# Kernel tuning notes

Measured on AMD Instinct MI355X. Metric: run time of the kernel, lower is better.

## Reference

```python
import jax, jax.numpy as jnp
import numpy as np

EMB = 1024
HEADS = 16
HEAD_DIM = EMB // HEADS
FF = 4 * EMB
EPS = 1e-5


def gelu_tanh(x):
    c = jnp.sqrt(jnp.asarray(2.0 / jnp.pi, dtype=x.dtype))
    return 0.5 * x * (1.0 + jnp.tanh(c * (x + 0.044715 * x ** 3)))


def layernorm(x, scale, bias):
    mean = jnp.mean(x, axis=-1, keepdims=True)
    # torch x.var() default is unbiased (ddof=1)
    var = jnp.var(x, axis=-1, keepdims=True, ddof=1)
    return (x - mean) / jnp.sqrt(var + EPS) * scale + bias


def setup_inputs() -> dict:
    key = jax.random.key(0)
    ks = jax.random.split(key, 12)
    s = lambda k, shape, sc=0.02: (jax.random.normal(k, shape, dtype=jnp.float32) * sc)
    return {
        "x": jax.random.normal(ks[0], (4, 2048, EMB), dtype=jnp.float32),
        "Wq": s(ks[1], (EMB, EMB)),
        "Wk": s(ks[2], (EMB, EMB)),
        "Wv": s(ks[3], (EMB, EMB)),
        "Wo": s(ks[4], (EMB, EMB)),
        "bo": jnp.zeros((EMB,), jnp.float32),
        "ln1_scale": jnp.ones((EMB,), jnp.float32),
        "ln1_bias": jnp.zeros((EMB,), jnp.float32),
        "ln2_scale": jnp.ones((EMB,), jnp.float32),
        "ln2_bias": jnp.zeros((EMB,), jnp.float32),
        "W1": s(ks[5], (EMB, FF)),
        "b1": jnp.zeros((FF,), jnp.float32),
        "W2": s(ks[6], (FF, EMB)),
        "b2": jnp.zeros((EMB,), jnp.float32),
    }


def reference(x, Wq, Wk, Wv, Wo, bo, ln1_scale, ln1_bias, ln2_scale, ln2_bias, W1, b1, W2, b2):
    b, n, _ = x.shape
    # --- attention sub-block (pre-LN) ---
    h = layernorm(x, ln1_scale, ln1_bias)
    q = (h @ Wq).reshape(b, n, HEADS, HEAD_DIM).transpose(0, 2, 1, 3)  # b,h,s,d
    k = (h @ Wk).reshape(b, n, HEADS, HEAD_DIM).transpose(0, 2, 1, 3)
    v = (h @ Wv).reshape(b, n, HEADS, HEAD_DIM).transpose(0, 2, 1, 3)
    scores = jnp.einsum("bhqd,bhkd->bhqk", q, k)
    causal = jnp.tril(jnp.ones((n, n), dtype=bool))
    scores = jnp.where(causal, scores, -jnp.inf)
    attn = jax.nn.softmax(scores / jnp.sqrt(jnp.asarray(HEAD_DIM, scores.dtype)), axis=-1)
    ctx = jnp.einsum("bhqk,bhkd->bhqd", attn, v).transpose(0, 2, 1, 3).reshape(b, n, EMB)
    attn_out = ctx @ Wo + bo
    x = x + attn_out  # dropout = identity (eval)
    # --- MLP sub-block ---
    h = layernorm(x, ln2_scale, ln2_bias)
    h = gelu_tanh(h @ W1 + b1) @ W2 + b2
    return x + h
```

## Files before the change

kernel.cpp:

```cpp
#include <hip/hip_runtime.h>
#include <hip/hip_bf16.h>
#include <math.h>

typedef __hip_bfloat16 bf16;
typedef __attribute__((ext_vector_type(8))) short short8;
typedef __attribute__((ext_vector_type(4))) float floatx4;

#define EMB   1024
#define SEQ   2048
#define BATCH 4
#define M_TOK 8192
#define HEADS 16
#define HDIM  64
#define FFDIM 4096
#define KVB   64

typedef __attribute__((address_space(3))) void lds_t;
typedef __attribute__((address_space(1))) void glob_t;

static __device__ __forceinline__ void gll16(const bf16* g, bf16* l) {
  __builtin_amdgcn_global_load_lds((const glob_t*)g, (lds_t*)l, 16, 0, 0);
}

static __device__ __forceinline__ unsigned short f2bu(float f) {
  union { __hip_bfloat16 h; unsigned short u; } cv;
  cv.h = __float2bfloat16(f);
  return cv.u;
}

static __device__ __forceinline__ float gelu_f(float x) {
  float t = tanhf(0.7978845608028654f * (x + 0.044715f * x * x * x));
  return 0.5f * x * (1.0f + t);
}

__global__ __launch_bounds__(256) void wconv_kernel(const float* __restrict__ W,
                                                    bf16* __restrict__ Wt,
                                                    int Kd, int Nd) {
  __shared__ float tile[32][33];
  int n0 = blockIdx.x * 32, k0 = blockIdx.y * 32;
  int tx = threadIdx.x & 31, ty = threadIdx.x >> 5;
  #pragma unroll
  for (int j = 0; j < 32; j += 8)
    tile[ty + j][tx] = W[(size_t)(k0 + ty + j) * Nd + n0 + tx];
  __syncthreads();
  #pragma unroll
  for (int j = 0; j < 32; j += 8)
    Wt[(size_t)(n0 + ty + j) * Kd + k0 + tx] = __float2bfloat16(tile[tx][ty + j]);
}

__global__ __launch_bounds__(256) void ln_kernel(const float* __restrict__ x,
                                                 const float* __restrict__ sc,
                                                 const float* __restrict__ bi,
                                                 bf16* __restrict__ out) {
  int row = blockIdx.x, tid = threadIdx.x;
  const float4* xr = (const float4*)(x + (size_t)row * EMB);
  float4 v = xr[tid];
  float s  = v.x + v.y + v.z + v.w;
  float s2 = v.x * v.x + v.y * v.y + v.z * v.z + v.w * v.w;
  #pragma unroll
  for (int off = 1; off < 64; off <<= 1) {
    s  += __shfl_xor(s, off);
    s2 += __shfl_xor(s2, off);
  }
  __shared__ float red[8];
  int wv = tid >> 6;
  if ((tid & 63) == 0) { red[wv] = s; red[4 + wv] = s2; }
  __syncthreads();
  s  = red[0] + red[1] + red[2] + red[3];
  s2 = red[4] + red[5] + red[6] + red[7];
  float mean = s * (1.0f / EMB);
  float var  = (s2 - (float)EMB * mean * mean) * (1.0f / (EMB - 1));
  float rstd = rsqrtf(var + 1e-5f);
  float4 scv = ((const float4*)sc)[tid];
  float4 biv = ((const float4*)bi)[tid];
  ushort4 o;
  o.x = f2bu((v.x - mean) * rstd * scv.x + biv.x);
  o.y = f2bu((v.y - mean) * rstd * scv.y + biv.y);
  o.z = f2bu((v.z - mean) * rstd * scv.z + biv.z);
  o.w = f2bu((v.w - mean) * rstd * scv.w + biv.w);
  ((ushort4*)(out + (size_t)row * EMB))[tid] = o;
}

template<int Kd, int MODE>
__global__ __launch_bounds__(256, 4) void gemm2_kernel(
    const bf16* __restrict__ A, const bf16* __restrict__ Bt,
    const float* __restrict__ bias, const float* __restrict__ resid,
    void* __restrict__ outp) {
  constexpr int NT = Kd / 32;
  __shared__ __align__(16) bf16 As[2][128 * 32];
  __shared__ __align__(16) bf16 Bs[2][128 * 32];
  const int tid = threadIdx.x;
  const int lane = tid & 63, wave = tid >> 6;
  const int lo = lane & 15, hi = lane >> 4;
  const int wr = wave >> 1, wc = wave & 1;
  const int m0 = blockIdx.x * 128, n0 = blockIdx.y * 128;

  const bf16* Bt2 = Bt;
  if constexpr (MODE == 6) Bt2 = Bt + ((size_t)blockIdx.z << 20);
  const bf16* Ab = A   + (size_t)m0 * Kd;
  const bf16* Bb = Bt2 + (size_t)n0 * Kd;

  auto STAGE = [&](int t, int b) {
    #pragma unroll
    for (int s = 0; s < 2; ++s) {
      const int c = tid + s * 256;
      const int row = c >> 2, slot = (c & 3) ^ (row & 3);
      gll16(Ab + (size_t)row * Kd + t * 32 + slot * 8, As[b] + c * 8);
      gll16(Bb + (size_t)row * Kd + t * 32 + slot * 8, Bs[b] + c * 8);
    }
  };

  floatx4 acc[4][4];
  #pragma unroll
  for (int i = 0; i < 4; i++)
    #pragma unroll
    for (int j = 0; j < 4; j++)
      #pragma unroll
      for (int r = 0; r < 4; r++) acc[i][j][r] = 0.0f;

  STAGE(0, 0);

  for (int t = 0; t < NT; ++t) {
    const int bb = t & 1;
    __builtin_amdgcn_s_barrier();
    __builtin_amdgcn_sched_barrier(0);
    if (t + 1 < NT) {
      STAGE(t + 1, bb ^ 1);
      asm volatile("s_waitcnt vmcnt(4)" ::: "memory");
    } else {
      asm volatile("s_waitcnt vmcnt(0)" ::: "memory");
    }
    __builtin_amdgcn_sched_barrier(0);
    short8 af[4], bfr[4];
    #pragma unroll
    for (int i = 0; i < 4; i++) {
      const int row = wr * 64 + i * 16 + lo;
      af[i] = *(const short8*)&As[bb][row * 32 + ((hi ^ (lo & 3)) * 8)];
    }
    #pragma unroll
    for (int j = 0; j < 4; j++) {
      const int row = wc * 64 + j * 16 + lo;
      bfr[j] = *(const short8*)&Bs[bb][row * 32 + ((hi ^ (lo & 3)) * 8)];
    }
    __builtin_amdgcn_s_setprio(1);
    #pragma unroll
    for (int i = 0; i < 4; i++)
      #pragma unroll
      for (int j = 0; j < 4; j++)
        acc[i][j] = __builtin_amdgcn_mfma_f32_16x16x32_bf16(af[i], bfr[j], acc[i][j], 0, 0, 0);
    __builtin_amdgcn_s_setprio(0);
  }

  #pragma unroll
  for (int i = 0; i < 4; i++) {
    #pragma unroll
    for (int j = 0; j < 4; j++) {
      const int mb = m0 + wr * 64 + i * 16 + hi * 4;
      const int n  = n0 + wc * 64 + j * 16 + lo;
      if constexpr (MODE == 6) {
        const int z = blockIdx.z;
        const int bx = mb >> 11, hhh = n >> 6, d = n & 63;
        bf16* ob = (bf16*)outp + ((size_t)z << 23);
        if (z == 2) {
          ushort4 pk;
          pk.x = f2bu(acc[i][j][0]); pk.y = f2bu(acc[i][j][1]);
          pk.z = f2bu(acc[i][j][2]); pk.w = f2bu(acc[i][j][3]);
          *(ushort4*)&ob[((size_t)(bx * HEADS + hhh) * HDIM + d) * SEQ + (mb & 2047)] = pk;
        } else {
          const float sc = (z == 0) ? 0.125f : 1.0f;
          #pragma unroll
          for (int r = 0; r < 4; r++) {
            const int ss = (mb + r) & 2047;
            ob[((size_t)(bx * HEADS + hhh) * SEQ + ss) * HDIM + d] =
                __float2bfloat16(acc[i][j][r] * sc);
          }
        }
      } else if constexpr (MODE == 3) {
        #pragma unroll
        for (int r = 0; r < 4; r++) {
          const int m = mb + r;
          ((float*)outp)[(size_t)m * EMB + n] =
              acc[i][j][r] + bias[n] + resid[(size_t)m * EMB + n];
        }
      } else if constexpr (MODE == 4) {
        #pragma unroll
        for (int r = 0; r < 4; r++)
          ((bf16*)outp)[(size_t)(mb + r) * FFDIM + n] =
              __float2bfloat16(gelu_f(acc[i][j][r] + bias[n]));
      }
    }
  }
}

__global__ __launch_bounds__(256, 2) void attn_kernel(
    const bf16* __restrict__ q, const bf16* __restrict__ k,
    const bf16* __restrict__ vt, bf16* __restrict__ ctx) {
  __shared__ __align__(16) char KVs[2][2][64 * 128];
  __shared__ __align__(16) char Pls[4][4096];
  const int bh = blockIdx.x, qt = blockIdx.y;
  const int tid = threadIdx.x;
  const int wave = tid >> 6, lane = tid & 63;
  const int lo = lane & 15, hi = lane >> 4;
  const int lo7 = lo & 7;
  const int q0 = qt * 128;
  const int q0w = q0 + wave * 32;
  const int qmax = q0w + 31;

  const bf16* qp = q  + ((size_t)bh * SEQ + q0w) * HDIM;
  const bf16* kp = k  + (size_t)bh * SEQ * HDIM;
  const bf16* vp = vt + (size_t)bh * HDIM * SEQ;

  short8 qf[2][2];
  #pragma unroll
  for (int m = 0; m < 2; m++)
    #pragma unroll
    for (int kk = 0; kk < 2; kk++)
      qf[m][kk] = *(const short8*)&qp[(size_t)(m * 16 + lo) * HDIM + kk * 32 + hi * 8];

  float m_run[2] = {-1e30f, -1e30f};
  float l_run[2] = {0.0f, 0.0f};
  floatx4 o[4][2];
  #pragma unroll
  for (int df = 0; df < 4; df++)
    #pragma unroll
    for (int m = 0; m < 2; m++)
      #pragma unroll
      for (int r = 0; r < 4; r++) o[df][m][r] = 0.0f;

  const int nt = 2 * qt + 2;

  const int c0 = tid, c1 = tid + 256;
  const int r0 = c0 >> 3, s0 = (c0 & 7) ^ (r0 & 7);
  const int r1 = c1 >> 3, s1 = (c1 & 7) ^ (r1 & 7);

  gll16(kp + (size_t)r0 * HDIM + s0 * 8, (bf16*)&KVs[0][0][c0 * 16]);
  gll16(vp + (size_t)r0 * SEQ + s0 * 8,  (bf16*)&KVs[0][1][c0 * 16]);
  gll16(kp + (size_t)r1 * HDIM + s1 * 8, (bf16*)&KVs[0][0][c1 * 16]);
  gll16(vp + (size_t)r1 * SEQ + s1 * 8,  (bf16*)&KVs[0][1][c1 * 16]);

  for (int t = 0; t < nt; ++t) {
    const int buf = t & 1;
    const int k0 = t * KVB;
    if (t + 1 < nt) {
      const int kn = k0 + KVB;
      gll16(kp + (size_t)(kn + r0) * HDIM + s0 * 8, (bf16*)&KVs[buf ^ 1][0][c0 * 16]);
      gll16(vp + (size_t)r0 * SEQ + kn + s0 * 8,    (bf16*)&KVs[buf ^ 1][1][c0 * 16]);
      gll16(kp + (size_t)(kn + r1) * HDIM + s1 * 8, (bf16*)&KVs[buf ^ 1][0][c1 * 16]);
      gll16(vp + (size_t)r1 * SEQ + kn + s1 * 8,    (bf16*)&KVs[buf ^ 1][1][c1 * 16]);
      asm volatile("s_waitcnt vmcnt(4)" ::: "memory");
    } else {
      asm volatile("s_waitcnt vmcnt(0)" ::: "memory");
    }
    __builtin_amdgcn_s_barrier();
    __builtin_amdgcn_sched_barrier(0);

    if (k0 <= qmax) {
      const char* Kb = KVs[buf][0];
      const char* Vb = KVs[buf][1];
      floatx4 sfr[4][2];
      __builtin_amdgcn_s_setprio(1);
      #pragma unroll
      for (int kf = 0; kf < 4; kf++) {
        const int rowb = (kf * 16 + lo) * 128;
        short8 kf0 = *(const short8*)(Kb + rowb + (( 0 + hi * 16) ^ (lo7 << 4)));
        short8 kf1 = *(const short8*)(Kb + rowb + ((64 + hi * 16) ^ (lo7 << 4)));
        #pragma unroll
        for (int m = 0; m < 2; m++) {
          floatx4 z = {0.0f, 0.0f, 0.0f, 0.0f};
          z = __builtin_amdgcn_mfma_f32_16x16x32_bf16(kf0, qf[m][0], z, 0, 0, 0);
          z = __builtin_amdgcn_mfma_f32_16x16x32_bf16(kf1, qf[m][1], z, 0, 0, 0);
          sfr[kf][m] = z;
        }
      }
      __builtin_amdgcn_s_setprio(0);
      if (k0 + KVB - 1 > q0w) {
        #pragma unroll
        for (int m = 0; m < 2; m++) {
          const int qg = q0w + m * 16 + lo;
          #pragma unroll
          for (int kf = 0; kf < 4; kf++)
            #pragma unroll
            for (int r = 0; r < 4; r++) {
              const int key = k0 + kf * 16 + hi * 4 + r;
              if (key > qg) sfr[kf][m][r] = -1e30f;
            }
        }
      }
      float alpha[2];
      #pragma unroll
      for (int m = 0; m < 2; m++) {
        float tmax = -1e30f;
        #pragma unroll
        for (int kf = 0; kf < 4; kf++)
          #pragma unroll
          for (int r = 0; r < 4; r++) tmax = fmaxf(tmax, sfr[kf][m][r]);
        tmax = fmaxf(tmax, __shfl_xor(tmax, 16));
        tmax = fmaxf(tmax, __shfl_xor(tmax, 32));
        const float mn = fmaxf(m_run[m], tmax);
        alpha[m] = __expf(m_run[m] - mn);
        m_run[m] = mn;
        float ps = 0.0f;
        const int prow = (m * 16 + lo) * 128;
        #pragma unroll
        for (int kf = 0; kf < 4; kf++) {
          float p0 = __expf(sfr[kf][m][0] - mn);
          float p1 = __expf(sfr[kf][m][1] - mn);
          float p2 = __expf(sfr[kf][m][2] - mn);
          float p3 = __expf(sfr[kf][m][3] - mn);
          ps += (p0 + p1) + (p2 + p3);
          ushort4 pk;
          pk.x = f2bu(p0); pk.y = f2bu(p1); pk.z = f2bu(p2); pk.w = f2bu(p3);
          *(ushort4*)(Pls[wave] + prow + ((kf * 32 + hi * 8) ^ (lo7 << 4))) = pk;
        }
        ps += __shfl_xor(ps, 16);
        ps += __shfl_xor(ps, 32);
        l_run[m] = l_run[m] * alpha[m] + ps;
      }
      asm volatile("s_waitcnt lgkmcnt(0)" ::: "memory");
      __builtin_amdgcn_sched_barrier(0);
      short8 pa[2][2];
      #pragma unroll
      for (int m = 0; m < 2; m++)
        #pragma unroll
        for (int kk2 = 0; kk2 < 2; kk2++)
          pa[m][kk2] = *(const short8*)(Pls[wave] + (m * 16 + lo) * 128 +
                                        ((kk2 * 64 + hi * 16) ^ (lo7 << 4)));
      float ar[2][4];
      #pragma unroll
      for (int m = 0; m < 2; m++)
        #pragma unroll
        for (int r = 0; r < 4; r++) ar[m][r] = __shfl(alpha[m], hi * 4 + r);
      #pragma unroll
      for (int df = 0; df < 4; df++)
        #pragma unroll
        for (int m = 0; m < 2; m++)
          #pragma unroll
          for (int r = 0; r < 4; r++) o[df][m][r] *= ar[m][r];
      __builtin_amdgcn_s_setprio(1);
      #pragma unroll
      for (int df = 0; df < 4; df++) {
        const int rowb = (df * 16 + lo) * 128;
        short8 vf0 = *(const short8*)(Vb + rowb + (( 0 + hi * 16) ^ (lo7 << 4)));
        short8 vf1 = *(const short8*)(Vb + rowb + ((64 + hi * 16) ^ (lo7 << 4)));
        #pragma unroll
        for (int m = 0; m < 2; m++) {
          o[df][m] = __builtin_amdgcn_mfma_f32_16x16x32_bf16(pa[m][0], vf0, o[df][m], 0, 0, 0);
          o[df][m] = __builtin_amdgcn_mfma_f32_16x16x32_bf16(pa[m][1], vf1, o[df][m], 0, 0, 0);
        }
      }
      __builtin_amdgcn_s_setprio(0);
    }
    __builtin_amdgcn_s_barrier();
    __builtin_amdgcn_sched_barrier(0);
  }

  const int b = bh >> 4, hh = bh & 15;
  #pragma unroll
  for (int m = 0; m < 2; m++) {
    float lr[4];
    #pragma unroll
    for (int r = 0; r < 4; r++) lr[r] = __shfl(l_run[m], hi * 4 + r);
    #pragma unroll
    for (int df = 0; df < 4; df++)
      #pragma unroll
      for (int r = 0; r < 4; r++) {
        const int srow = q0w + m * 16 + hi * 4 + r;
        ctx[((size_t)(b * SEQ + srow)) * EMB + hh * HDIM + df * 16 + lo] =
            __float2bfloat16(o[df][m][r] / lr[r]);
      }
  }
}

extern "C" void kernel_launch(void* const* d_in, const int* in_sizes, int n_in,
                              void* d_out, int out_size, void* d_ws, size_t ws_size,
                              hipStream_t stream) {
  const float* x   = (const float*)d_in[0];
  const float* Wq  = (const float*)d_in[1];
  const float* Wk  = (const float*)d_in[2];
  const float* Wv  = (const float*)d_in[3];
  const float* Wo  = (const float*)d_in[4];
  const float* bo  = (const float*)d_in[5];
  const float* l1s = (const float*)d_in[6];
  const float* l1b = (const float*)d_in[7];
  const float* l2s = (const float*)d_in[8];
  const float* l2b = (const float*)d_in[9];
  const float* W1  = (const float*)d_in[10];
  const float* b1  = (const float*)d_in[11];
  const float* W2  = (const float*)d_in[12];
  const float* b2  = (const float*)d_in[13];
  float* out = (float*)d_out;

  char* ws = (char*)d_ws;
  bf16* hbuf   = (bf16*)(ws);
  bf16* qbuf   = (bf16*)(ws + ((size_t)16 << 20));
  bf16* kbuf   = (bf16*)(ws + ((size_t)32 << 20));
  bf16* vbuf   = (bf16*)(ws + ((size_t)48 << 20));
  bf16* ctxbuf = hbuf;
  bf16* gbuf   = (bf16*)(ws);
  bf16* h2buf  = (bf16*)(ws + ((size_t)64 << 20));
  bf16* WqT    = (bf16*)(ws + ((size_t)80 << 20));
  bf16* WkT    = WqT + (1u << 20);
  bf16* WvT    = WkT + (1u << 20);
  bf16* WoT    = WvT + (1u << 20);
  bf16* W1T    = WoT + (1u << 20);
  bf16* W2T    = W1T + (4u << 20);

  wconv_kernel<<<dim3(32, 32), 256, 0, stream>>>(Wq, WqT, 1024, 1024);
  wconv_kernel<<<dim3(32, 32), 256, 0, stream>>>(Wk, WkT, 1024, 1024);
  wconv_kernel<<<dim3(32, 32), 256, 0, stream>>>(Wv, WvT, 1024, 1024);
  wconv_kernel<<<dim3(32, 32), 256, 0, stream>>>(Wo, WoT, 1024, 1024);
  wconv_kernel<<<dim3(128, 32), 256, 0, stream>>>(W1, W1T, 1024, 4096);
  wconv_kernel<<<dim3(32, 128), 256, 0, stream>>>(W2, W2T, 4096, 1024);

  ln_kernel<<<8192, 256, 0, stream>>>(x, l1s, l1b, hbuf);

  gemm2_kernel<1024, 6><<<dim3(64, 8, 3), 256, 0, stream>>>(
      hbuf, WqT, nullptr, nullptr, qbuf);

  attn_kernel<<<dim3(64, 16), 256, 0, stream>>>(qbuf, kbuf, vbuf, ctxbuf);

  gemm2_kernel<1024, 3><<<dim3(64, 8), 256, 0, stream>>>(
      ctxbuf, WoT, bo, x, (void*)out);
  ln_kernel<<<8192, 256, 0, stream>>>(out, l2s, l2b, h2buf);
  gemm2_kernel<1024, 4><<<dim3(64, 32), 256, 0, stream>>>(
      h2buf, W1T, b1, nullptr, gbuf);
  gemm2_kernel<4096, 3><<<dim3(64, 8), 256, 0, stream>>>(
      gbuf, W2T, b2, out, (void*)out);
}
```

Before: 519.1 us.

## Fuse weight conversions, unroll GEMM k-loop with precomputed pointers, cheaper GELU

The six weight-transpose launches become a single launch that picks the matrix from a flattened block index. The GEMM main loop is unrolled by two with fixed buffer indices and incremented global pointers, so per-iteration address arithmetic goes away. The LDS swizzle changes from row&3 to (row>>1)&3, applied on both the store and load sides, to alter bank-conflict behaviour. GELU's tanh is rewritten as an exp-based sigmoid form, which is mathematically equivalent but uses the fast __expf intrinsic.

After: 516.9 us. About the same (-0.4%).

```diff
diff --git a/kernel.cpp b/kernel.cpp
--- a/kernel.cpp
+++ b/kernel.cpp
@@ -29,16 +29,30 @@
 }
 
 static __device__ __forceinline__ float gelu_f(float x) {
-  float t = tanhf(0.7978845608028654f * (x + 0.044715f * x * x * x));
-  return 0.5f * x * (1.0f + t);
-}
-
-__global__ __launch_bounds__(256) void wconv_kernel(const float* __restrict__ W,
-                                                    bf16* __restrict__ Wt,
-                                                    int Kd, int Nd) {
+  float y = 0.7978845608028654f * (x + 0.044715f * x * x * x);
+  return x / (1.0f + __expf(-2.0f * y));
+}
+
+__global__ __launch_bounds__(256) void wconv_all_kernel(
+    const float* __restrict__ Wq, const float* __restrict__ Wk,
+    const float* __restrict__ Wv, const float* __restrict__ Wo,
+    const float* __restrict__ W1, const float* __restrict__ W2,
+    bf16* WqT, bf16* WkT, bf16* WvT, bf16* WoT, bf16* W1T, bf16* W2T) {
+  const int idx = blockIdx.x;
+  const float* W; bf16* Wt; int Kd, Nd, rem;
+  if (idx < 4096) {
+    const int m = idx >> 10; rem = idx & 1023; Kd = 1024; Nd = 1024;
+    W  = (m == 0) ? Wq  : (m == 1) ? Wk  : (m == 2) ? Wv  : Wo;
+    Wt = (m == 0) ? WqT : (m == 1) ? WkT : (m == 2) ? WvT : WoT;
+  } else if (idx < 8192) {
+    rem = idx - 4096; Kd = 1024; Nd = 4096; W = W1; Wt = W1T;
+  } else {
+    rem = idx - 8192; Kd = 4096; Nd = 1024; W = W2; Wt = W2T;
+  }
+  const int nb = Nd >> 5;
+  const int n0 = (rem % nb) * 32, k0 = (rem / nb) * 32;
   __shared__ float tile[32][33];
-  int n0 = blockIdx.x * 32, k0 = blockIdx.y * 32;
-  int tx = threadIdx.x & 31, ty = threadIdx.x >> 5;
+  const int tx = threadIdx.x & 31, ty = threadIdx.x >> 5;
   #pragma unroll
   for (int j = 0; j < 32; j += 8)
     tile[ty + j][tx] = W[(size_t)(k0 + ty + j) * Nd + n0 + tx];
@@ -100,15 +114,14 @@
   const bf16* Ab = A   + (size_t)m0 * Kd;
   const bf16* Bb = Bt2 + (size_t)n0 * Kd;
 
-  auto STAGE = [&](int t, int b) {
-    #pragma unroll
-    for (int s = 0; s < 2; ++s) {
-      const int c = tid + s * 256;
-      const int row = c >> 2, slot = (c & 3) ^ (row & 3);
-      gll16(Ab + (size_t)row * Kd + t * 32 + slot * 8, As[b] + c * 8);
-      gll16(Bb + (size_t)row * Kd + t * 32 + slot * 8, Bs[b] + c * 8);
-    }
-  };
+  const int c0 = tid, c1 = tid + 256;
+  const int ssw = (tid & 3) ^ ((tid >> 3) & 3);
+  const bf16* pa0 = Ab + (size_t)(c0 >> 2) * Kd + ssw * 8;
+  const bf16* pa1 = Ab + (size_t)(c1 >> 2) * Kd + ssw * 8;
+  const bf16* pb0 = Bb + (size_t)(c0 >> 2) * Kd + ssw * 8;
+  const bf16* pb1 = Bb + (size_t)(c1 >> 2) * Kd + ssw * 8;
+
+  const int koff = (hi ^ ((lo >> 1) & 3)) * 8;
 
   floatx4 acc[4][4];
   #pragma unroll
@@ -118,14 +131,17 @@
       #pragma unroll
       for (int r = 0; r < 4; r++) acc[i][j][r] = 0.0f;
 
-  STAGE(0, 0);
-
-  for (int t = 0; t < NT; ++t) {
-    const int bb = t & 1;
+  gll16(pa0, As[0] + c0 * 8); gll16(pb0, Bs[0] + c0 * 8);
+  gll16(pa1, As[0] + c1 * 8); gll16(pb1, Bs[0] + c1 * 8);
+  pa0 += 32; pb0 += 32; pa1 += 32; pb1 += 32;
+
+  auto KSTEP = [&](int bb, bool stage_next) {
     __builtin_amdgcn_s_barrier();
     __builtin_amdgcn_sched_barrier(0);
-    if (t + 1 < NT) {
-      STAGE(t + 1, bb ^ 1);
+    if (stage_next) {
+      gll16(pa0, As[bb ^ 1] + c0 * 8); gll16(pb0, Bs[bb ^ 1] + c0 * 8);
+      gll16(pa1, As[bb ^ 1] + c1 * 8); gll16(pb1, Bs[bb ^ 1] + c1 * 8);
+      pa0 += 32; pb0 += 32; pa1 += 32; pb1 += 32;
       asm volatile("s_waitcnt vmcnt(4)" ::: "memory");
     } else {
       asm volatile("s_waitcnt vmcnt(0)" ::: "memory");
@@ -133,15 +149,11 @@
     __builtin_amdgcn_sched_barrier(0);
     short8 af[4], bfr[4];
     #pragma unroll
-    for (int i = 0; i < 4; i++) {
-      const int row = wr * 64 + i * 16 + lo;
-      af[i] = *(const short8*)&As[bb][row * 32 + ((hi ^ (lo & 3)) * 8)];
-    }
-    #pragma unroll
-    for (int j = 0; j < 4; j++) {
-      const int row = wc * 64 + j * 16 + lo;
-      bfr[j] = *(const short8*)&Bs[bb][row * 32 + ((hi ^ (lo & 3)) * 8)];
-    }
+    for (int i = 0; i < 4; i++)
+      af[i] = *(const short8*)&As[bb][(wr * 64 + i * 16 + lo) * 32 + koff];
+    #pragma unroll
+    for (int j = 0; j < 4; j++)
+      bfr[j] = *(const short8*)&Bs[bb][(wc * 64 + j * 16 + lo) * 32 + koff];
     __builtin_amdgcn_s_setprio(1);
     #pragma unroll
     for (int i = 0; i < 4; i++)
@@ -149,6 +161,11 @@
       for (int j = 0; j < 4; j++)
         acc[i][j] = __builtin_amdgcn_mfma_f32_16x16x32_bf16(af[i], bfr[j], acc[i][j], 0, 0, 0);
     __builtin_amdgcn_s_setprio(0);
+  };
+
+  for (int t = 0; t < NT; t += 2) {
+    KSTEP(0, t + 1 < NT);
+    KSTEP(1, t + 2 < NT);
   }
 
   #pragma unroll
@@ -405,12 +422,8 @@
   bf16* W1T    = WoT + (1u << 20);
   bf16* W2T    = W1T + (4u << 20);
 
-  wconv_kernel<<<dim3(32, 32), 256, 0, stream>>>(Wq, WqT, 1024, 1024);
-  wconv_kernel<<<dim3(32, 32), 256, 0, stream>>>(Wk, WkT, 1024, 1024);
-  wconv_kernel<<<dim3(32, 32), 256, 0, stream>>>(Wv, WvT, 1024, 1024);
-  wconv_kernel<<<dim3(32, 32), 256, 0, stream>>>(Wo, WoT, 1024, 1024);
-  wconv_kernel<<<dim3(128, 32), 256, 0, stream>>>(W1, W1T, 1024, 4096);
-  wconv_kernel<<<dim3(32, 128), 256, 0, stream>>>(W2, W2T, 4096, 1024);
+  wconv_all_kernel<<<12288, 256, 0, stream>>>(Wq, Wk, Wv, Wo, W1, W2,
+                                              WqT, WkT, WvT, WoT, W1T, W2T);
 
   ln_kernel<<<8192, 256, 0, stream>>>(x, l1s, l1b, hbuf);
 
```
